# Kernel tuning notes

Hardware: AMD Instinct MI355X
Metric: run time of the kernel (lower is better)

## Reference

```python
import jax, jax.numpy as jnp
import numpy as np

E = 29          # number of cell types (TRAINING_CELL_TYPES)
D = 1985        # input gene dim
B = 32768       # batch of cells
ENC = [512, 256, 256]
EPS = 1e-5


def setup_inputs() -> dict:
    key = jax.random.key(0)
    ks = jax.random.split(key, 16)
    inp = {}
    inp["x"] = jax.random.normal(ks[0], (B, D), dtype=jnp.float32)
    inp["labels"] = jax.random.randint(ks[1], (B,), 0, E, dtype=jnp.int32)
    # shared encoder: Linear -> BatchNorm(eval: running stats) -> ReLU, 3 layers
    dims = [D] + ENC
    ki = 2
    for l in range(3):
        fi, fo = dims[l], dims[l + 1]
        inp[f"W{l}"] = jax.random.normal(ks[ki], (fi, fo), jnp.float32) / np.sqrt(fi).astype(np.float32); ki += 1
        inp[f"b{l}"] = jnp.zeros((fo,), jnp.float32)
        inp[f"g{l}"] = jnp.ones((fo,), jnp.float32)    # BN gamma
        inp[f"be{l}"] = jnp.zeros((fo,), jnp.float32)  # BN beta
        inp[f"m{l}"] = jnp.zeros((fo,), jnp.float32)   # BN running mean
        inp[f"v{l}"] = jnp.ones((fo,), jnp.float32)    # BN running var
    # 29 stacked per-cell-type heads: 256 -> 128 -> 64 -> 1 (LayerNorm+ReLU between)
    inp["HW1"] = jax.random.normal(ks[ki], (E, 256, 128), jnp.float32) / 16.0; ki += 1
    inp["Hb1"] = jnp.zeros((E, 128), jnp.float32)
    inp["LG1"] = jnp.ones((E, 128), jnp.float32)
    inp["LB1"] = jnp.zeros((E, 128), jnp.float32)
    inp["HW2"] = jax.random.normal(ks[ki], (E, 128, 64), jnp.float32) / np.sqrt(128).astype(np.float32); ki += 1
    inp["Hb2"] = jnp.zeros((E, 64), jnp.float32)
    inp["LG2"] = jnp.ones((E, 64), jnp.float32)
    inp["LB2"] = jnp.zeros((E, 64), jnp.float32)
    inp["HWo"] = jax.random.normal(ks[ki], (E, 64), jnp.float32) / 8.0; ki += 1
    inp["Hbo"] = jnp.zeros((E,), jnp.float32)
    return inp


def _ln(h, g, b):
    mu = h.mean(-1, keepdims=True)
    var = h.var(-1, keepdims=True)
    return (h - mu) / jnp.sqrt(var + EPS) * g + b


def reference(x, labels,
              W0, b0, g0, be0, m0, v0,
              W1, b1, g1, be1, m1, v1,
              W2, b2, g2, be2, m2, v2,
              HW1, Hb1, LG1, LB1, HW2, Hb2, LG2, LB2, HWo, Hbo):
    # shared encoder (eval-mode BatchNorm, dropout off)
    h = x
    for W, bb, g, be, m, v in ((W0, b0, g0, be0, m0, v0),
                               (W1, b1, g1, be1, m1, v1),
                               (W2, b2, g2, be2, m2, v2)):
        h = h @ W + bb
        h = (h - m) / jnp.sqrt(v + EPS) * g + be
        h = jax.nn.relu(h)
    feats = h  # [B, 256]
    # all-expert dense compute (identical math to per-group routing), then select
    t = jnp.einsum('bd,edh->ebh', feats, HW1) + Hb1[:, None, :]     # [E,B,128]
    t = jax.nn.relu(_ln(t, LG1[:, None, :], LB1[:, None, :]))
    t = jnp.einsum('ebh,ehk->ebk', t, HW2) + Hb2[:, None, :]        # [E,B,64]
    t = jax.nn.relu(_ln(t, LG2[:, None, :], LB2[:, None, :]))
    out_all = jnp.einsum('ebk,ek->eb', t, HWo) + Hbo[:, None]       # [E,B]
    preds = jnp.take_along_axis(out_all, labels[None, :].astype(jnp.int32), axis=0)[0]  # [B]
    return preds
```

## Files before the change

### kernel.cpp

```cpp
#include <hip/hip_runtime.h>
#include <hip/hip_bf16.h>


typedef __bf16 bf16_t;
typedef bf16_t bf16x8 __attribute__((ext_vector_type(8)));
typedef float  f32x4  __attribute__((ext_vector_type(4)));

#define LDK 40
#define MAX_TILES 544
#define T1_LD 136

__global__ __launch_bounds__(256) void repack_x(const float* __restrict__ x,
                                                bf16_t* __restrict__ xp) {
    const unsigned idx = blockIdx.x * 256u + threadIdx.x;
    const unsigned r = idx / 2016u;
    const unsigned c = idx % 2016u;
    float v = (c < 1985u) ? x[(size_t)r * 1985u + c] : 0.f;
    xp[idx] = (bf16_t)v;
}

__global__ __launch_bounds__(256) void prep_bn(const float* __restrict__ b,
                                               const float* __restrict__ g,
                                               const float* __restrict__ be,
                                               const float* __restrict__ m,
                                               const float* __restrict__ v,
                                               float* __restrict__ s,
                                               float* __restrict__ b2, int N) {
    int n = blockIdx.x * 256 + threadIdx.x;
    if (n < N) {
        float sv = g[n] * rsqrtf(v[n] + 1e-5f);
        s[n]  = sv;
        b2[n] = (b[n] - m[n]) * sv + be[n];
    }
}

__global__ __launch_bounds__(256) void transpose_scale_pad(const float* __restrict__ in,
                                                           bf16_t* __restrict__ out,
                                                           const float* __restrict__ scale,
                                                           int K, int N, int Kp, int total) {
    const unsigned tid = blockIdx.x * 256u + threadIdx.x;
    if (tid >= (unsigned)total) return;
    const unsigned kchunks = (unsigned)Kp / 8u;
    const unsigned bn = tid / kchunks;
    const unsigned kc = tid % kchunks;
    const unsigned b  = bn / (unsigned)N;
    const unsigned n  = bn % (unsigned)N;
    const unsigned k0 = kc * 8u;
    const float sc = scale ? scale[n] : 1.f;
    bf16x8 v{};
#pragma unroll
    for (int j = 0; j < 8; ++j) {
        unsigned k = k0 + j;
        v[j] = (k < (unsigned)K)
                 ? (bf16_t)(in[((size_t)b * K + k) * N + n] * sc)
                 : (bf16_t)0.f;
    }
    *(bf16x8*)&out[((size_t)b * N + n) * Kp + k0] = v;
}

__global__ __launch_bounds__(256) void gemm_bias_relu(const bf16_t* __restrict__ A,
                                                      const bf16_t* __restrict__ Bt,
                                                      const float* __restrict__ bias,
                                                      bf16_t* __restrict__ C,
                                                      int M, int N, int K) {
    __shared__ bf16_t As[128 * LDK];
    __shared__ bf16_t Bs[128 * LDK];

    const int tid  = threadIdx.x;
    const int bm0  = blockIdx.y * 128;
    const int bn0  = blockIdx.x * 128;
    const int wave = tid >> 6, lane = tid & 63;
    const int wm   = (wave & 1) * 64, wn = (wave >> 1) * 64;
    const int quad = lane >> 4, tq = lane & 15;

    f32x4 acc[4][4] = {};

    const int r0 = tid >> 2;
    const int c0 = (tid & 3) * 8;

    const bf16_t* Ap0 = A + (size_t)(bm0 + r0) * K + c0;
    const bf16_t* Ap1 = A + (size_t)(bm0 + r0 + 64) * K + c0;
    const bf16_t* Bp0 = Bt + (size_t)(bn0 + r0) * K + c0;
    const bf16_t* Bp1 = Bt + (size_t)(bn0 + r0 + 64) * K + c0;

    bf16_t* AsW0 = &As[r0 * LDK + c0];
    bf16_t* AsW1 = &As[(r0 + 64) * LDK + c0];
    bf16_t* BsW0 = &Bs[r0 * LDK + c0];
    bf16_t* BsW1 = &Bs[(r0 + 64) * LDK + c0];

    for (int k0 = 0; k0 < K; k0 += 32) {
        bf16x8 a0 = *(const bf16x8*)(Ap0 + k0);
        bf16x8 a1 = *(const bf16x8*)(Ap1 + k0);
        bf16x8 b0 = *(const bf16x8*)(Bp0 + k0);
        bf16x8 b1 = *(const bf16x8*)(Bp1 + k0);
        __syncthreads();
        *(bf16x8*)AsW0 = a0;
        *(bf16x8*)AsW1 = a1;
        *(bf16x8*)BsW0 = b0;
        *(bf16x8*)BsW1 = b1;
        __syncthreads();

        bf16x8 af[4], bfr[4];
#pragma unroll
        for (int mt = 0; mt < 4; ++mt)
            af[mt] = *(const bf16x8*)&As[(wm + mt * 16 + tq) * LDK + quad * 8];
#pragma unroll
        for (int nt = 0; nt < 4; ++nt)
            bfr[nt] = *(const bf16x8*)&Bs[(wn + nt * 16 + tq) * LDK + quad * 8];
#pragma unroll
        for (int mt = 0; mt < 4; ++mt)
#pragma unroll
            for (int nt = 0; nt < 4; ++nt)
                acc[mt][nt] = __builtin_amdgcn_mfma_f32_16x16x32_bf16(
                    af[mt], bfr[nt], acc[mt][nt], 0, 0, 0);
    }

#pragma unroll
    for (int nt = 0; nt < 4; ++nt) {
        const int col = bn0 + wn + nt * 16 + tq;
        const float bcol = bias[col];
#pragma unroll
        for (int mt = 0; mt < 4; ++mt) {
#pragma unroll
            for (int r = 0; r < 4; ++r) {
                const int row = bm0 + wm + mt * 16 + quad * 4 + r;
                float v = acc[mt][nt][r] + bcol;
                v = v > 0.f ? v : 0.f;
                C[(size_t)row * N + col] = (bf16_t)v;
            }
        }
    }
}

__global__ __launch_bounds__(64) void head_init(int* __restrict__ counts) {
    if (threadIdx.x < 32) counts[threadIdx.x] = 0;
}

__global__ __launch_bounds__(256) void head_hist(const int* __restrict__ labels,
                                                 int* __restrict__ counts) {
    __shared__ int h[32];
    if (threadIdx.x < 32) h[threadIdx.x] = 0;
    __syncthreads();
    int c = blockIdx.x * 256 + threadIdx.x;
    atomicAdd(&h[labels[c]], 1);
    __syncthreads();
    if (threadIdx.x < 32) {
        int v = h[threadIdx.x];
        if (v) atomicAdd(&counts[threadIdx.x], v);
    }
}

__global__ __launch_bounds__(1024) void head_plan(const int* __restrict__ counts,
                                                  int* __restrict__ cursor,
                                                  int4* __restrict__ descs) {
    __shared__ int offs[30];
    __shared__ int toffs[30];
    if (threadIdx.x == 0) {
        int off = 0, toff = 0;
        for (int e = 0; e < 29; ++e) {
            offs[e] = off; toffs[e] = toff;
            int n = counts[e];
            off += n; toff += (n + 63) >> 6;
        }
        offs[29] = off; toffs[29] = toff;
    }
    __syncthreads();
    if (threadIdx.x < 29) cursor[threadIdx.x] = offs[threadIdx.x];
    int t = threadIdx.x;
    if (t < MAX_TILES) {
        int4 d = make_int4(0, 0, 0, 0);
        if (t < toffs[29]) {
            int e = 0;
            while (toffs[e + 1] <= t) ++e;
            int ti = t - toffs[e];
            int n  = counts[e];
            d.x = e;
            d.y = offs[e] + ti * 64;
            d.z = min(64, n - ti * 64);
        }
        descs[t] = d;
    }
}

__global__ __launch_bounds__(256) void head_scatter(const int* __restrict__ labels,
                                                    int* __restrict__ cursor,
                                                    int* __restrict__ perm) {
    int c = blockIdx.x * 256 + threadIdx.x;
    int p = atomicAdd(&cursor[labels[c]], 1);
    perm[p] = c;
}

__global__ __launch_bounds__(256) void head_mfma(const bf16_t* __restrict__ feats,
                                                 const int* __restrict__ perm,
                                                 const int4* __restrict__ descs,
                                                 const bf16_t* __restrict__ HW1t,
                                                 const float* __restrict__ Hb1,
                                                 const float* __restrict__ LG1,
                                                 const float* __restrict__ LB1,
                                                 const bf16_t* __restrict__ HW2t,
                                                 const float* __restrict__ Hb2,
                                                 const float* __restrict__ LG2,
                                                 const float* __restrict__ LB2,
                                                 const float* __restrict__ HWo,
                                                 const float* __restrict__ Hbo,
                                                 float* __restrict__ out) {
    __shared__ bf16_t t1s[64 * T1_LD];

    const int4 d = descs[blockIdx.x];
    const int e = d.x, start = d.y, count = d.z;
    if (count == 0) return;

    const int tid = threadIdx.x, w = tid >> 6, lane = tid & 63;
    const int tq = lane & 15, quad = lane >> 4;
    const int m0 = w * 16;

    const int am = m0 + tq;
    const int ridx = perm[start + ((am < count) ? am : 0)];
    const bf16_t* arow = feats + (size_t)ridx * 256;

    const bf16_t* w1 = HW1t + (size_t)e * 128 * 256;
    f32x4 acc1[8] = {};
#pragma unroll
    for (int ks = 0; ks < 8; ++ks) {
        bf16x8 a = *(const bf16x8*)(arow + ks * 32 + quad * 8);
#pragma unroll
        for (int nt = 0; nt < 8; ++nt) {
            bf16x8 b = *(const bf16x8*)(w1 + (size_t)(nt * 16 + tq) * 256 + ks * 32 + quad * 8);
            acc1[nt] = __builtin_amdgcn_mfma_f32_16x16x32_bf16(a, b, acc1[nt], 0, 0, 0);
        }
    }

    float s1[4] = {}, q1[4] = {};
#pragma unroll
    for (int nt = 0; nt < 8; ++nt) {
        float hb = Hb1[e * 128 + nt * 16 + tq];
#pragma unroll
        for (int r = 0; r < 4; ++r) {
            float v = acc1[nt][r] + hb;
            acc1[nt][r] = v;
            s1[r] += v; q1[r] += v * v;
        }
    }
#pragma unroll
    for (int off = 1; off < 16; off <<= 1)
#pragma unroll
        for (int r = 0; r < 4; ++r) {
            s1[r] += __shfl_xor(s1[r], off);
            q1[r] += __shfl_xor(q1[r], off);
        }
    float mu1[4], rs1[4];
#pragma unroll
    for (int r = 0; r < 4; ++r) {
        mu1[r] = s1[r] * (1.f / 128.f);
        rs1[r] = rsqrtf(q1[r] * (1.f / 128.f) - mu1[r] * mu1[r] + 1e-5f);
    }
#pragma unroll
    for (int nt = 0; nt < 8; ++nt) {
        const int col = nt * 16 + tq;
        const float lg = LG1[e * 128 + col], lb = LB1[e * 128 + col];
#pragma unroll
        for (int r = 0; r < 4; ++r) {
            float t = (acc1[nt][r] - mu1[r]) * rs1[r] * lg + lb;
            t1s[(m0 + quad * 4 + r) * T1_LD + col] = (bf16_t)fmaxf(t, 0.f);
        }
    }
    __syncthreads();

    const bf16_t* w2 = HW2t + (size_t)e * 64 * 128;
    f32x4 acc2[4] = {};
#pragma unroll
    for (int ks = 0; ks < 4; ++ks) {
        bf16x8 a = *(const bf16x8*)&t1s[(m0 + tq) * T1_LD + ks * 32 + quad * 8];
#pragma unroll
        for (int nt = 0; nt < 4; ++nt) {
            bf16x8 b = *(const bf16x8*)(w2 + (size_t)(nt * 16 + tq) * 128 + ks * 32 + quad * 8);
            acc2[nt] = __builtin_amdgcn_mfma_f32_16x16x32_bf16(a, b, acc2[nt], 0, 0, 0);
        }
    }

    float s2[4] = {}, q2[4] = {};
#pragma unroll
    for (int nt = 0; nt < 4; ++nt) {
        float hb = Hb2[e * 64 + nt * 16 + tq];
#pragma unroll
        for (int r = 0; r < 4; ++r) {
            float v = acc2[nt][r] + hb;
            acc2[nt][r] = v;
            s2[r] += v; q2[r] += v * v;
        }
    }
#pragma unroll
    for (int off = 1; off < 16; off <<= 1)
#pragma unroll
        for (int r = 0; r < 4; ++r) {
            s2[r] += __shfl_xor(s2[r], off);
            q2[r] += __shfl_xor(q2[r], off);
        }
    float p[4] = {};
#pragma unroll
    for (int nt = 0; nt < 4; ++nt) {
        const int col = nt * 16 + tq;
        const float lg = LG2[e * 64 + col], lb = LB2[e * 64 + col];
        const float wo = HWo[e * 64 + col];
#pragma unroll
        for (int r = 0; r < 4; ++r) {
            float mu = s2[r] * (1.f / 64.f);
            float rs = rsqrtf(q2[r] * (1.f / 64.f) - mu * mu + 1e-5f);
            float t = (acc2[nt][r] - mu) * rs * lg + lb;
            p[r] += fmaxf(t, 0.f) * wo;
        }
    }
#pragma unroll
    for (int off = 1; off < 16; off <<= 1)
#pragma unroll
        for (int r = 0; r < 4; ++r) p[r] += __shfl_xor(p[r], off);

    if (tq == 0) {
        const float hbo = Hbo[e];
#pragma unroll
        for (int r = 0; r < 4; ++r) {
            int m = m0 + quad * 4 + r;
            if (m < count) out[perm[start + m]] = p[r] + hbo;
        }
    }
}

static const size_t OFF_XP    = 0;
static const size_t OFF_H1    = 0;
static const size_t OFF_FEATS = 16777216;
static const size_t OFF_H0    = 132120576;
static const size_t OFF_CNT   = 132120576;
static const size_t OFF_CUR   = 132120832;
static const size_t OFF_DESC  = 132121088;
static const size_t OFF_PERM  = 132136960;
static const size_t OFF_WT0   = 165675008;
static const size_t OFF_WT1   = 167739392;
static const size_t OFF_WT2   = 168001536;
static const size_t OFF_B20   = 168132608;
static const size_t OFF_B21   = 168134656;
static const size_t OFF_B22   = 168135680;
static const size_t OFF_S0    = 168136704;
static const size_t OFF_S1    = 168138752;
static const size_t OFF_S2    = 168139776;
static const size_t OFF_HW1T  = 168140800;
static const size_t OFF_HW2T  = 170041344;

extern "C" void kernel_launch(void* const* d_in, const int* in_sizes, int n_in,
                              void* d_out, int out_size, void* d_ws, size_t ws_size,
                              hipStream_t stream) {
    const float* x      = (const float*)d_in[0];
    const int*   labels = (const int*)d_in[1];
    const float* W[3]   = {(const float*)d_in[2], (const float*)d_in[8],  (const float*)d_in[14]};
    const float* bb[3]  = {(const float*)d_in[3], (const float*)d_in[9],  (const float*)d_in[15]};
    const float* g[3]   = {(const float*)d_in[4], (const float*)d_in[10], (const float*)d_in[16]};
    const float* be[3]  = {(const float*)d_in[5], (const float*)d_in[11], (const float*)d_in[17]};
    const float* mm[3]  = {(const float*)d_in[6], (const float*)d_in[12], (const float*)d_in[18]};
    const float* vv[3]  = {(const float*)d_in[7], (const float*)d_in[13], (const float*)d_in[19]};
    const float* HW1 = (const float*)d_in[20];
    const float* Hb1 = (const float*)d_in[21];
    const float* LG1 = (const float*)d_in[22];
    const float* LB1 = (const float*)d_in[23];
    const float* HW2 = (const float*)d_in[24];
    const float* Hb2 = (const float*)d_in[25];
    const float* LG2 = (const float*)d_in[26];
    const float* LB2 = (const float*)d_in[27];
    const float* HWo = (const float*)d_in[28];
    const float* Hbo = (const float*)d_in[29];

    char* ws = (char*)d_ws;
    bf16_t* xp    = (bf16_t*)(ws + OFF_XP);
    bf16_t* h0    = (bf16_t*)(ws + OFF_H0);
    bf16_t* h1    = (bf16_t*)(ws + OFF_H1);
    bf16_t* feats = (bf16_t*)(ws + OFF_FEATS);
    bf16_t* Wt[3] = {(bf16_t*)(ws + OFF_WT0), (bf16_t*)(ws + OFF_WT1), (bf16_t*)(ws + OFF_WT2)};
    float*  b2[3] = {(float*)(ws + OFF_B20), (float*)(ws + OFF_B21), (float*)(ws + OFF_B22)};
    float*  sc[3] = {(float*)(ws + OFF_S0), (float*)(ws + OFF_S1), (float*)(ws + OFF_S2)};
    bf16_t* HW1t  = (bf16_t*)(ws + OFF_HW1T);
    bf16_t* HW2t  = (bf16_t*)(ws + OFF_HW2T);
    int*    cnt   = (int*)(ws + OFF_CNT);
    int*    cur   = (int*)(ws + OFF_CUR);
    int4*   descs = (int4*)(ws + OFF_DESC);
    int*    perm  = (int*)(ws + OFF_PERM);
    float*  outp  = (float*)d_out;

    repack_x<<<258048, 256, 0, stream>>>(x, xp);

    prep_bn<<<2, 256, 0, stream>>>(bb[0], g[0], be[0], mm[0], vv[0], sc[0], b2[0], 512);
    prep_bn<<<1, 256, 0, stream>>>(bb[1], g[1], be[1], mm[1], vv[1], sc[1], b2[1], 256);
    prep_bn<<<1, 256, 0, stream>>>(bb[2], g[2], be[2], mm[2], vv[2], sc[2], b2[2], 256);
    transpose_scale_pad<<<504, 256, 0, stream>>>(W[0], Wt[0], sc[0], 1985, 512, 2016, 129024);
    transpose_scale_pad<<<64,  256, 0, stream>>>(W[1], Wt[1], sc[1], 512, 256, 512, 16384);
    transpose_scale_pad<<<32,  256, 0, stream>>>(W[2], Wt[2], sc[2], 256, 256, 256, 8192);
    transpose_scale_pad<<<464, 256, 0, stream>>>(HW1, HW1t, nullptr, 256, 128, 256, 118784);
    transpose_scale_pad<<<116, 256, 0, stream>>>(HW2, HW2t, nullptr, 128, 64, 128, 29696);

    dim3 blk(256);
    dim3 grid0(512 / 128, 32768 / 128);
    gemm_bias_relu<<<grid0, blk, 0, stream>>>(xp, Wt[0], b2[0], h0, 32768, 512, 2016);
    dim3 grid1(256 / 128, 32768 / 128);
    gemm_bias_relu<<<grid1, blk, 0, stream>>>(h0, Wt[1], b2[1], h1, 32768, 256, 512);

    head_init<<<1, 64, 0, stream>>>(cnt);
    head_hist<<<128, 256, 0, stream>>>(labels, cnt);
    head_plan<<<1, 1024, 0, stream>>>(cnt, cur, descs);
    head_scatter<<<128, 256, 0, stream>>>(labels, cur, perm);

    gemm_bias_relu<<<grid1, blk, 0, stream>>>(h1, Wt[2], b2[2], feats, 32768, 256, 256);

    head_mfma<<<MAX_TILES, 256, 0, stream>>>(feats, perm, descs, HW1t, Hb1, LG1, LB1,
                                             HW2t, Hb2, LG2, LB2, HWo, Hbo, outp);
}
```

Before: 778.2 us.

## Fuse x fp32-to-bf16 conversion into first GEMM, batch prep kernels, swizzle LDS

Drops the separate repack pass over the 32768x1985 fp32 input. The first GEMM now reads fp32 x directly, converts it to bf16 on load, and zero-masks the padded K tail. The small BN-prep and weight-transpose launches are merged into two kernels, and the padded LDS layout is replaced by an XOR swizzle to avoid bank conflicts. The risk is that the fp32 loads in the GEMM are scalar, unaligned rows (stride 1985), which may hurt load throughput in the GEMM main loop.

```diff
diff --git a/kernel.cpp b/kernel.cpp
--- a/kernel.cpp
+++ b/kernel.cpp
@@ -6,43 +6,37 @@
 typedef bf16_t bf16x8 __attribute__((ext_vector_type(8)));
 typedef float  f32x4  __attribute__((ext_vector_type(4)));
 
-#define LDK 40
 #define MAX_TILES 544
 #define T1_LD 136
 
-__global__ __launch_bounds__(256) void repack_x(const float* __restrict__ x,
-                                                bf16_t* __restrict__ xp) {
-    const unsigned idx = blockIdx.x * 256u + threadIdx.x;
-    const unsigned r = idx / 2016u;
-    const unsigned c = idx % 2016u;
-    float v = (c < 1985u) ? x[(size_t)r * 1985u + c] : 0.f;
-    xp[idx] = (bf16_t)v;
-}
-
-__global__ __launch_bounds__(256) void prep_bn(const float* __restrict__ b,
-                                               const float* __restrict__ g,
-                                               const float* __restrict__ be,
-                                               const float* __restrict__ m,
-                                               const float* __restrict__ v,
-                                               float* __restrict__ s,
-                                               float* __restrict__ b2, int N) {
-    int n = blockIdx.x * 256 + threadIdx.x;
-    if (n < N) {
-        float sv = g[n] * rsqrtf(v[n] + 1e-5f);
-        s[n]  = sv;
-        b2[n] = (b[n] - m[n]) * sv + be[n];
-    }
-}
-
-__global__ __launch_bounds__(256) void transpose_scale_pad(const float* __restrict__ in,
-                                                           bf16_t* __restrict__ out,
-                                                           const float* __restrict__ scale,
-                                                           int K, int N, int Kp, int total) {
-    const unsigned tid = blockIdx.x * 256u + threadIdx.x;
-    if (tid >= (unsigned)total) return;
+__global__ __launch_bounds__(256) void prep_bn_all(
+    const float* __restrict__ b0, const float* __restrict__ g0, const float* __restrict__ be0,
+    const float* __restrict__ m0, const float* __restrict__ v0,
+    const float* __restrict__ b1, const float* __restrict__ g1, const float* __restrict__ be1,
+    const float* __restrict__ m1, const float* __restrict__ v1,
+    const float* __restrict__ b2i, const float* __restrict__ g2, const float* __restrict__ be2,
+    const float* __restrict__ m2, const float* __restrict__ v2,
+    float* __restrict__ s0, float* __restrict__ o0,
+    float* __restrict__ s1, float* __restrict__ o1,
+    float* __restrict__ s2, float* __restrict__ o2) {
+    const int bid = blockIdx.x, tid = threadIdx.x;
+    const float *b, *g, *be, *m, *v;
+    float *s, *o;
+    int n;
+    if (bid < 2)      { b = b0;  g = g0; be = be0; m = m0; v = v0; s = s0; o = o0; n = bid * 256 + tid; }
+    else if (bid == 2){ b = b1;  g = g1; be = be1; m = m1; v = v1; s = s1; o = o1; n = tid; }
+    else              { b = b2i; g = g2; be = be2; m = m2; v = v2; s = s2; o = o2; n = tid; }
+    float sv = g[n] * rsqrtf(v[n] + 1e-5f);
+    s[n] = sv;
+    o[n] = (b[n] - m[n]) * sv + be[n];
+}
+
+__device__ __forceinline__ void tsp_one(const float* __restrict__ in, bf16_t* __restrict__ out,
+                                        const float* __restrict__ scale,
+                                        int K, int N, int Kp, unsigned t) {
     const unsigned kchunks = (unsigned)Kp / 8u;
-    const unsigned bn = tid / kchunks;
-    const unsigned kc = tid % kchunks;
+    const unsigned bn = t / kchunks;
+    const unsigned kc = t % kchunks;
     const unsigned b  = bn / (unsigned)N;
     const unsigned n  = bn % (unsigned)N;
     const unsigned k0 = kc * 8u;
@@ -51,20 +45,34 @@
 #pragma unroll
     for (int j = 0; j < 8; ++j) {
         unsigned k = k0 + j;
-        v[j] = (k < (unsigned)K)
-                 ? (bf16_t)(in[((size_t)b * K + k) * N + n] * sc)
-                 : (bf16_t)0.f;
+        v[j] = (k < (unsigned)K) ? (bf16_t)(in[((size_t)b * K + k) * N + n] * sc)
+                                 : (bf16_t)0.f;
     }
     *(bf16x8*)&out[((size_t)b * N + n) * Kp + k0] = v;
 }
 
-__global__ __launch_bounds__(256) void gemm_bias_relu(const bf16_t* __restrict__ A,
+__global__ __launch_bounds__(256) void prep_weights(
+    const float* __restrict__ W0, const float* __restrict__ W1, const float* __restrict__ W2,
+    const float* __restrict__ HW1, const float* __restrict__ HW2,
+    const float* __restrict__ s0, const float* __restrict__ s1, const float* __restrict__ s2,
+    bf16_t* __restrict__ Wt0, bf16_t* __restrict__ Wt1, bf16_t* __restrict__ Wt2,
+    bf16_t* __restrict__ HW1t, bf16_t* __restrict__ HW2t) {
+    unsigned t = blockIdx.x * 256u + threadIdx.x;
+    if      (t < 129024u) tsp_one(W0,  Wt0,  s0, 1985, 512, 2016, t);
+    else if (t < 145408u) tsp_one(W1,  Wt1,  s1, 512,  256, 512,  t - 129024u);
+    else if (t < 153600u) tsp_one(W2,  Wt2,  s2, 256,  256, 256,  t - 145408u);
+    else if (t < 272384u) tsp_one(HW1, HW1t, nullptr, 256, 128, 256, t - 153600u);
+    else                  tsp_one(HW2, HW2t, nullptr, 128, 64,  128, t - 272384u);
+}
+
+template<bool AF32>
+__global__ __launch_bounds__(256) void gemm_bias_relu(const void* __restrict__ Av,
                                                       const bf16_t* __restrict__ Bt,
                                                       const float* __restrict__ bias,
                                                       bf16_t* __restrict__ C,
-                                                      int M, int N, int K) {
-    __shared__ bf16_t As[128 * LDK];
-    __shared__ bf16_t Bs[128 * LDK];
+                                                      int M, int N, int K, int KA) {
+    __shared__ bf16_t As[128 * 32];
+    __shared__ bf16_t Bs[128 * 32];
 
     const int tid  = threadIdx.x;
     const int bm0  = blockIdx.y * 128;
@@ -72,25 +80,45 @@
     const int wave = tid >> 6, lane = tid & 63;
     const int wm   = (wave & 1) * 64, wn = (wave >> 1) * 64;
     const int quad = lane >> 4, tq = lane & 15;
+    const int xq   = (quad ^ (tq & 3)) << 3;
 
     f32x4 acc[4][4] = {};
 
     const int r0 = tid >> 2;
-    const int c0 = (tid & 3) * 8;
-
-    const bf16_t* Ap0 = A + (size_t)(bm0 + r0) * K + c0;
-    const bf16_t* Ap1 = A + (size_t)(bm0 + r0 + 64) * K + c0;
+    const int j0 = tid & 3;
+    const int c0 = j0 * 8;
+    const int sw = ((j0 ^ (r0 & 3)) << 3);
+
+    bf16_t* AsW0 = &As[ r0       * 32 + sw];
+    bf16_t* AsW1 = &As[(r0 + 64) * 32 + sw];
+    bf16_t* BsW0 = &Bs[ r0       * 32 + sw];
+    bf16_t* BsW1 = &Bs[(r0 + 64) * 32 + sw];
+
+    const bf16_t* Ab = (const bf16_t*)Av;
+    const float*  Af = (const float*)Av;
     const bf16_t* Bp0 = Bt + (size_t)(bn0 + r0) * K + c0;
     const bf16_t* Bp1 = Bt + (size_t)(bn0 + r0 + 64) * K + c0;
 
-    bf16_t* AsW0 = &As[r0 * LDK + c0];
-    bf16_t* AsW1 = &As[(r0 + 64) * LDK + c0];
-    bf16_t* BsW0 = &Bs[r0 * LDK + c0];
-    bf16_t* BsW1 = &Bs[(r0 + 64) * LDK + c0];
-
     for (int k0 = 0; k0 < K; k0 += 32) {
-        bf16x8 a0 = *(const bf16x8*)(Ap0 + k0);
-        bf16x8 a1 = *(const bf16x8*)(Ap1 + k0);
+        bf16x8 a0, a1;
+        if constexpr (AF32) {
+            const float* sA0 = Af + (size_t)(bm0 + r0) * KA + k0 + c0;
+            const float* sA1 = Af + (size_t)(bm0 + r0 + 64) * KA + k0 + c0;
+            if (k0 + 32 <= KA) {
+#pragma unroll
+                for (int j = 0; j < 8; ++j) { a0[j] = (bf16_t)sA0[j]; a1[j] = (bf16_t)sA1[j]; }
+            } else {
+#pragma unroll
+                for (int j = 0; j < 8; ++j) {
+                    bool ok = (k0 + c0 + j) < KA;
+                    a0[j] = ok ? (bf16_t)sA0[j] : (bf16_t)0.f;
+                    a1[j] = ok ? (bf16_t)sA1[j] : (bf16_t)0.f;
+                }
+            }
+        } else {
+            a0 = *(const bf16x8*)(Ab + (size_t)(bm0 + r0) * K + k0 + c0);
+            a1 = *(const bf16x8*)(Ab + (size_t)(bm0 + r0 + 64) * K + k0 + c0);
+        }
         bf16x8 b0 = *(const bf16x8*)(Bp0 + k0);
         bf16x8 b1 = *(const bf16x8*)(Bp1 + k0);
         __syncthreads();
@@ -103,10 +131,10 @@
         bf16x8 af[4], bfr[4];
 #pragma unroll
         for (int mt = 0; mt < 4; ++mt)
-            af[mt] = *(const bf16x8*)&As[(wm + mt * 16 + tq) * LDK + quad * 8];
+            af[mt] = *(const bf16x8*)&As[(wm + mt * 16 + tq) * 32 + xq];
 #pragma unroll
         for (int nt = 0; nt < 4; ++nt)
-            bfr[nt] = *(const bf16x8*)&Bs[(wn + nt * 16 + tq) * LDK + quad * 8];
+            bfr[nt] = *(const bf16x8*)&Bs[(wn + nt * 16 + tq) * 32 + xq];
 #pragma unroll
         for (int mt = 0; mt < 4; ++mt)
 #pragma unroll
@@ -325,25 +353,24 @@
     }
 }
 
-static const size_t OFF_XP    = 0;
-static const size_t OFF_H1    = 0;
-static const size_t OFF_FEATS = 16777216;
-static const size_t OFF_H0    = 132120576;
-static const size_t OFF_CNT   = 132120576;
-static const size_t OFF_CUR   = 132120832;
-static const size_t OFF_DESC  = 132121088;
-static const size_t OFF_PERM  = 132136960;
-static const size_t OFF_WT0   = 165675008;
-static const size_t OFF_WT1   = 167739392;
-static const size_t OFF_WT2   = 168001536;
-static const size_t OFF_B20   = 168132608;
-static const size_t OFF_B21   = 168134656;
-static const size_t OFF_B22   = 168135680;
-static const size_t OFF_S0    = 168136704;
-static const size_t OFF_S1    = 168138752;
-static const size_t OFF_S2    = 168139776;
-static const size_t OFF_HW1T  = 168140800;
-static const size_t OFF_HW2T  = 170041344;
+static const size_t OFF_H0    = 0;
+static const size_t OFF_H1    = 33554432;
+static const size_t OFF_FEATS = 50331648;
+static const size_t OFF_WT0   = 67108864;
+static const size_t OFF_WT1   = 69173248;
+static const size_t OFF_WT2   = 69435392;
+static const size_t OFF_HW1T  = 69566464;
+static const size_t OFF_HW2T  = 71467008;
+static const size_t OFF_B20   = 71942144;
+static const size_t OFF_B21   = 71944192;
+static const size_t OFF_B22   = 71945216;
+static const size_t OFF_S0    = 71946240;
+static const size_t OFF_S1    = 71948288;
+static const size_t OFF_S2    = 71949312;
+static const size_t OFF_CNT   = 71950336;
+static const size_t OFF_CUR   = 71950464;
+static const size_t OFF_DESC  = 71950592;
+static const size_t OFF_PERM  = 71959296;
 
 extern "C" void kernel_launch(void* const* d_in, const int* in_sizes, int n_in,
                               void* d_out, int out_size, void* d_ws, size_t ws_size,
@@ -368,44 +395,44 @@
     const float* Hbo = (const float*)d_in[29];
 
     char* ws = (char*)d_ws;
-    bf16_t* xp    = (bf16_t*)(ws + OFF_XP);
     bf16_t* h0    = (bf16_t*)(ws + OFF_H0);
     bf16_t* h1    = (bf16_t*)(ws + OFF_H1);
     bf16_t* feats = (bf16_t*)(ws + OFF_FEATS);
-    bf16_t* Wt[3] = {(bf16_t*)(ws + OFF_WT0), (bf16_t*)(ws + OFF_WT1), (bf16_t*)(ws + OFF_WT2)};
-    float*  b2[3] = {(float*)(ws + OFF_B20), (float*)(ws + OFF_B21), (float*)(ws + OFF_B22)};
-    float*  sc[3] = {(float*)(ws + OFF_S0), (float*)(ws + OFF_S1), (float*)(ws + OFF_S2)};
+    bf16_t* Wt0   = (bf16_t*)(ws + OFF_WT0);
+    bf16_t* Wt1   = (bf16_t*)(ws + OFF_WT1);
+    bf16_t* Wt2   = (bf16_t*)(ws + OFF_WT2);
     bf16_t* HW1t  = (bf16_t*)(ws + OFF_HW1T);
     bf16_t* HW2t  = (bf16_t*)(ws + OFF_HW2T);
+    float*  b20   = (float*)(ws + OFF_B20);
+    float*  b21   = (float*)(ws + OFF_B21);
+    float*  b22   = (float*)(ws + OFF_B22);
+    float*  s0    = (float*)(ws + OFF_S0);
+    float*  s1    = (float*)(ws + OFF_S1);
+    float*  s2    = (float*)(ws + OFF_S2);
     int*    cnt   = (int*)(ws + OFF_CNT);
     int*    cur   = (int*)(ws + OFF_CUR);
     int4*   descs = (int4*)(ws + OFF_DESC);
     int*    perm  = (int*)(ws + OFF_PERM);
     float*  outp  = (float*)d_out;
 
-    repack_x<<<258048, 256, 0, stream>>>(x, xp);
-
-    prep_bn<<<2, 256, 0, stream>>>(bb[0], g[0], be[0], mm[0], vv[0], sc[0], b2[0], 512);
-    prep_bn<<<1, 256, 0, stream>>>(bb[1], g[1], be[1], mm[1], vv[1], sc[1], b2[1], 256);
-    prep_bn<<<1, 256, 0, stream>>>(bb[2], g[2], be[2], mm[2], vv[2], sc[2], b2[2], 256);
-    transpose_scale_pad<<<504, 256, 0, stream>>>(W[0], Wt[0], sc[0], 1985, 512, 2016, 129024);
-    transpose_scale_pad<<<64,  256, 0, stream>>>(W[1], Wt[1], sc[1], 512, 256, 512, 16384);
-    transpose_scale_pad<<<32,  256, 0, stream>>>(W[2], Wt[2], sc[2], 256, 256, 256, 8192);
-    transpose_scale_pad<<<464, 256, 0, stream>>>(HW1, HW1t, nullptr, 256, 128, 256, 118784);
-    transpose_scale_pad<<<116, 256, 0, stream>>>(HW2, HW2t, nullptr, 128, 64, 128, 29696);
-
-    dim3 blk(256);
-    dim3 grid0(512 / 128, 32768 / 128);
-    gemm_bias_relu<<<grid0, blk, 0, stream>>>(xp, Wt[0], b2[0], h0, 32768, 512, 2016);
-    dim3 grid1(256 / 128, 32768 / 128);
-    gemm_bias_relu<<<grid1, blk, 0, stream>>>(h0, Wt[1], b2[1], h1, 32768, 256, 512);
+    prep_bn_all<<<4, 256, 0, stream>>>(bb[0], g[0], be[0], mm[0], vv[0],
+                                       bb[1], g[1], be[1], mm[1], vv[1],
+                                       bb[2], g[2], be[2], mm[2], vv[2],
+                                       s0, b20, s1, b21, s2, b22);
+    prep_weights<<<1180, 256, 0, stream>>>(W[0], W[1], W[2], HW1, HW2,
+                                           s0, s1, s2, Wt0, Wt1, Wt2, HW1t, HW2t);
 
     head_init<<<1, 64, 0, stream>>>(cnt);
     head_hist<<<128, 256, 0, stream>>>(labels, cnt);
     head_plan<<<1, 1024, 0, stream>>>(cnt, cur, descs);
     head_scatter<<<128, 256, 0, stream>>>(labels, cur, perm);
 
-    gemm_bias_relu<<<grid1, blk, 0, stream>>>(h1, Wt[2], b2[2], feats, 32768, 256, 256);
+    dim3 blk(256);
+    dim3 grid0(512 / 128, 32768 / 128);
+    gemm_bias_relu<true><<<grid0, blk, 0, stream>>>(x, Wt0, b20, h0, 32768, 512, 2016, 1985);
+    dim3 grid1(256 / 128, 32768 / 128);
+    gemm_bias_relu<false><<<grid1, blk, 0, stream>>>(h0, Wt1, b21, h1, 32768, 256, 512, 512);
+    gemm_bias_relu<false><<<grid1, blk, 0, stream>>>(h1, Wt2, b22, feats, 32768, 256, 256, 256);
 
     head_mfma<<<MAX_TILES, 256, 0, stream>>>(feats, perm, descs, HW1t, Hb1, LG1, LB1,
                                              HW2t, Hb2, LG2, LB2, HWo, Hbo, outp);
```

After: 783.4 us. Within noise of the previous version (+0.7%).
